# Kernel tuning notes

Hardware: AMD Instinct MI355X
Metric: run time of the kernel (lower is better)

Reference implementation:

```python
import jax, jax.numpy as jnp
import numpy as np
import math

B, T, C, TF, N, DK = 4, 2048, 768, 128, 8, 96  # DK = max(C//8,16)

def _tau_init(Tw):
    alpha = 0.1 ** (1.0 / max(Tw - 1, 1))
    tau = -math.log(max(alpha, 1e-10))
    return math.log(math.exp(tau) - 1 + 1e-10)

def setup_inputs() -> dict:
    key = jax.random.key(0)
    ks = jax.random.split(key, 13)
    w = lambda k, shp: jax.random.normal(k, shp, jnp.float32) * 0.02
    return {
        'x': jax.random.normal(ks[0], (B, T, C), jnp.float32),
        'tau_gate': jnp.float32(_tau_init(max(T // 2, 4))),
        'tau_fast': jnp.float32(_tau_init(TF)),
        'tau_slow': jnp.float32(_tau_init(T)),
        'Wp': w(ks[1], (C, C)), 'bp': jnp.zeros((C,), jnp.float32),
        'Wxf': w(ks[2], (C, C)), 'bxf': jnp.full((C,), -0.5, jnp.float32),
        'Wxs': w(ks[3], (C, C)), 'bxs': jnp.full((C,), 0.5, jnp.float32),
        'Wcf': w(ks[4], (C, C)), 'Wcs': w(ks[5], (C, C)),
        'Wq': w(ks[6], (DK, C)), 'Wk': w(ks[7], (DK, C)),
        'Wfast': w(ks[8], (C, C)), 'bfast': jnp.zeros((C,), jnp.float32),
        'Wslow': w(ks[9], (C, C)), 'bslow': jnp.zeros((C,), jnp.float32),
        'Wsoma': w(ks[10], (C, C)), 'bsoma': jnp.zeros((C,), jnp.float32),
        'Wanc': w(ks[11], (C, C)), 'banc': jnp.zeros((C,), jnp.float32),
        'anchor_scales': jnp.linspace(1.5, -1.5, N).astype(jnp.float32),
        'blend_raw': jnp.zeros((1,), jnp.float32),
        'ln_g': jnp.ones((C,), jnp.float32), 'ln_b': jnp.zeros((C,), jnp.float32),
    }

def _lin(x, W, b=None):
    # torch Linear: y = x @ W.T + b, W is (out, in)
    y = jnp.einsum('btc,oc->bto', x, W)
    return y if b is None else y + b

def _ema(b, tau_raw):
    # exact h_t = alpha*h_{t-1} + b_t, h_{-1}=0 (same math as full causal conv with kernel alpha^j)
    alpha = jnp.exp(-jax.nn.softplus(tau_raw))
    def step(h, bt):
        h = alpha * h + bt
        return h, h
    _, hs = jax.lax.scan(step, jnp.zeros_like(b[:, 0, :]), jnp.swapaxes(b, 0, 1))
    return jnp.swapaxes(hs, 0, 1)  # (B,T,C)

def _forward(x, tau_gate, tau_fast, tau_slow, Wp, bp, Wxf, bxf, Wxs, bxs, Wcf, Wcs,
             Wq, Wk, Wfast, bfast, Wslow, bslow, Wsoma, bsoma, Wanc, banc,
             anchor_scales, blend_raw, ln_g, ln_b):
    x_proj = jnp.tanh(_lin(x, Wp, bp))
    ctx_gate = _ema(x, tau_gate)
    wg_f = jax.nn.sigmoid(_lin(x, Wxf, bxf) + _lin(ctx_gate, Wcf))
    wg_s = jax.nn.sigmoid(_lin(x, Wxs, bxs) + _lin(ctx_gate, Wcs))
    ctx_fast = _ema(x_proj * wg_f, tau_fast)
    ctx_slow = _ema(x_proj * wg_s, tau_slow)
    # F1 content gate: causal max-score sigmoid
    q = _lin(x, Wq)
    k = _lin(x, Wk)
    sc = jnp.einsum('btd,bsd->bts', q, k) * (DK ** -0.5)
    tril = jnp.tril(jnp.ones((T, T), bool))
    sc = jnp.where(tril[None], sc, -jnp.inf)
    cg = jax.nn.sigmoid(jnp.max(sc, axis=-1, keepdims=True))  # (B,T,1)
    ctx_fast = ctx_fast * cg
    ctx_slow = ctx_slow * cg
    # F5 anchors (static positions)
    pos = np.array([min(i * (T // N), T - 1) for i in range(N)])
    a = jnp.tanh(jnp.einsum('bnc,oc->bno', x[:, pos, :], Wanc) + banc)  # (B,N,C)
    delta = jnp.einsum('n,bnc->bc', jax.nn.sigmoid(anchor_scales), a)
    ctx_fast = ctx_fast + delta[:, None, :]
    ctx_slow = ctx_slow + delta[:, None, :]
    # F6 blend of fast/slow gates (torch.lerp)
    bl = jax.nn.sigmoid(blend_raw)  # (1,)
    gf = jax.nn.sigmoid(_lin(ctx_fast, Wfast, bfast))
    gs = jax.nn.sigmoid(_lin(ctx_slow, Wslow, bslow))
    gate = gf + bl * (gs - gf)
    soma = jnp.tanh(_lin(x, Wsoma, bsoma))
    y = soma * gate
    mu = jnp.mean(y, -1, keepdims=True)
    var = jnp.var(y, -1, keepdims=True)
    return (y - mu) / jnp.sqrt(var + 1e-5) * ln_g + ln_b  # dropout p=0 -> identity

def reference(x, tau_gate, tau_fast, tau_slow, Wp, bp, Wxf, bxf, Wxs, bxs, Wcf, Wcs,
              Wq, Wk, Wfast, bfast, Wslow, bslow, Wsoma, bsoma, Wanc, banc,
              anchor_scales, blend_raw, ln_g, ln_b):
    return _forward(x, tau_gate, tau_fast, tau_slow, Wp, bp, Wxf, bxf, Wxs, bxs, Wcf, Wcs,
                    Wq, Wk, Wfast, bfast, Wslow, bslow, Wsoma, bsoma, Wanc, banc,
                    anchor_scales, blend_raw, ln_g, ln_b)
```

## Files before the change

### kernel.cpp

```cpp
#include <hip/hip_runtime.h>
#include <math.h>

#define B_ 4
#define T_ 2048
#define C_ 768
#define DK_ 96
#define NA_ 8
#define M_ (B_*T_)
#define K2_ (2*C_)
#define NCH_ 256
#define CK_ 8

typedef __attribute__((ext_vector_type(8))) _Float16 half8;
typedef __attribute__((ext_vector_type(4))) _Float16 half4;
typedef __attribute__((ext_vector_type(4))) float floatx4;

#define AS1 __attribute__((address_space(1)))
#define AS3 __attribute__((address_space(3)))

__device__ __forceinline__ float sigm(float x){ return 1.f/(1.f + expf(-x)); }
__device__ __forceinline__ unsigned enc_max(float f){
  unsigned i = __float_as_uint(f);
  return (i & 0x80000000u) ? ~i : (i | 0x80000000u);
}
__device__ __forceinline__ float dec_max(unsigned u){
  unsigned i = (u & 0x80000000u) ? (u & 0x7FFFFFFFu) : ~u;
  return __uint_as_float(i);
}
__device__ __forceinline__ void gld16(const _Float16* g, _Float16* l){
  __builtin_amdgcn_global_load_lds((const AS1 unsigned int*)g, (AS3 unsigned int*)l, 16, 0, 0);
}

#define NB0 4608
#define NB1 4896
#define NB2 5920
#define NB3 5944
__global__ __launch_bounds__(256) void k_prep(
    const float* __restrict__ x,
    const float* __restrict__ Wp, const float* __restrict__ Wfast,
    const float* __restrict__ Wslow, const float* __restrict__ Wsoma,
    const float* __restrict__ Wxf, const float* __restrict__ Wxs,
    const float* __restrict__ Wcf, const float* __restrict__ Wcs,
    const float* __restrict__ Wq, const float* __restrict__ Wk,
    const float* __restrict__ Wanc, const float* __restrict__ banc,
    const float* __restrict__ ascl, const float* __restrict__ tau_gate,
    _Float16* __restrict__ wall, _Float16* __restrict__ wqk,
    unsigned* __restrict__ cgE, _Float16* __restrict__ xh,
    float* __restrict__ Sg, float* __restrict__ dlt)
{
  __shared__ float xs[NA_*C_];
  __shared__ float part[NA_*128];
  int blk = blockIdx.x, tid = threadIdx.x;
  if (blk < NB0){
    int i = blk*256 + tid;
    const int per = (C_*C_)/4;
    int s = i / per, j = i - s*per;
    const float* src = s==0?Wp : s==1?Wfast : s==2?Wslow : s==3?Wsoma
                     : s==4?Wxf : s==5?Wxs : s==6?Wcf : Wcs;
    float4 v = ((const float4*)src)[j];
    half4 h = { (_Float16)v.x, (_Float16)v.y, (_Float16)v.z, (_Float16)v.w };
    ((half4*)wall)[(size_t)s*per + j] = h;
  } else if (blk < NB1){
    int sub = blk - NB0;
    if (sub >= 256){ cgE[(sub-256)*256 + tid] = 0u; return; }
    const float* src = (sub < 96) ? Wq + (size_t)sub*C_
                     : (sub < 192 ? Wk + (size_t)(sub-96)*C_ : nullptr);
    #pragma unroll
    for (int k = 0; k < 3; ++k){
      int c = tid + k*256;
      wqk[(size_t)sub*C_ + c] = src ? (_Float16)src[c] : (_Float16)0.f;
    }
  } else if (blk < NB2){
    if (tid >= 192) return;
    int sub = blk - NB1;
    float al = expf(-log1pf(expf(tau_gate[0])));
    int b = sub >> 8, ch = sub & (NCH_-1);
    int t0 = b*T_ + ch*CK_;
    float s0=0.f,s1=0.f,s2=0.f,s3=0.f;
    #pragma unroll
    for (int t = 0; t < CK_; ++t){
      float4 v = *(const float4*)(x + (size_t)(t0+t)*C_ + tid*4);
      half4 h = { (_Float16)v.x,(_Float16)v.y,(_Float16)v.z,(_Float16)v.w };
      *(half4*)(xh + (size_t)(t0+t)*C_ + tid*4) = h;
      s0 = al*s0 + v.x; s1 = al*s1 + v.y; s2 = al*s2 + v.z; s3 = al*s3 + v.w;
    }
    float4 sv = { s0,s1,s2,s3 };
    *(float4*)(Sg + (size_t)sub*C_ + tid*4) = sv;
  } else {
    int ab = blk - NB2;
    int ct = ab % 6, b = ab / 6;
    for (int i = tid; i < NA_*C_; i += 256){
      int n = i / C_, c = i - n*C_;
      xs[i] = x[(size_t)(b*T_ + n*(T_/NA_))*C_ + c];
    }
    __syncthreads();
    int col = ct*128 + (tid & 127), kh = tid >> 7;
    float acc[NA_] = {0,0,0,0,0,0,0,0};
    const float* wrow = Wanc + (size_t)col*C_ + kh*384;
    const float* xk = xs + kh*384;
    for (int k = 0; k < 384; ++k){
      float wv = wrow[k];
      #pragma unroll
      for (int n = 0; n < NA_; ++n) acc[n] += xk[n*C_ + k]*wv;
    }
    if (kh){
      #pragma unroll
      for (int n = 0; n < NA_; ++n) part[n*128 + (tid & 127)] = acc[n];
    }
    __syncthreads();
    if (!kh){
      float d = 0.f;
      float bv = banc[col];
      #pragma unroll
      for (int n = 0; n < NA_; ++n){
        float a = tanhf(acc[n] + part[n*128 + (tid & 127)] + bv);
        d += sigm(ascl[n]) * a;
      }
      dlt[(size_t)b*C_ + col] = d;
    }
  }
}

__global__ __launch_bounds__(256) void k_p2_gate(const float* __restrict__ S, float* __restrict__ H,
                                                 const float* __restrict__ tau){
  int blk = blockIdx.x;
  int b = blk / 3, c = (blk - b*3)*256 + threadIdx.x;
  float aCK = expf(-(float)CK_ * log1pf(expf(tau[0])));
  float h = 0.f;
  for (int ch = 0; ch < NCH_; ++ch){
    size_t idx = (size_t)(b*NCH_ + ch)*C_ + c;
    H[idx] = h;
    h = aCK*h + S[idx];
  }
}

__global__ __launch_bounds__(256) void k_p2_fs(const float* __restrict__ Sf, const float* __restrict__ Ss,
                                               float* __restrict__ Hf, float* __restrict__ Hs,
                                               const float* __restrict__ tf, const float* __restrict__ ts){
  int blk = blockIdx.x;
  int which = blk / 12, sub = blk - which*12;
  int b = sub / 3, c = (sub - b*3)*256 + threadIdx.x;
  const float* S = which ? Ss : Sf;
  float* H = which ? Hs : Hf;
  float aCK = expf(-(float)CK_ * log1pf(expf(which ? ts[0] : tf[0])));
  float h = 0.f;
  for (int ch = 0; ch < NCH_; ++ch){
    size_t idx = (size_t)(b*NCH_ + ch)*C_ + c;
    H[idx] = h;
    h = aCK*h + S[idx];
  }
}

__global__ __launch_bounds__(192) void k_gate_p3(
    const _Float16* __restrict__ xh, const float* __restrict__ H,
    const float* __restrict__ tau, _Float16* __restrict__ gate){
  float al = expf(-log1pf(expf(tau[0])));
  int blk = blockIdx.x, b = blk >> 8, ch = blk & (NCH_-1);
  int c4 = threadIdx.x;
  float4 h0 = *(const float4*)(H + (size_t)blk*C_ + c4*4);
  float g0=h0.x, g1=h0.y, g2=h0.z, g3=h0.w;
  int t0 = b*T_ + ch*CK_;
  #pragma unroll
  for (int t = 0; t < CK_; ++t){
    half4 v = *(const half4*)(xh + (size_t)(t0+t)*C_ + c4*4);
    g0 = al*g0 + (float)v[0]; g1 = al*g1 + (float)v[1];
    g2 = al*g2 + (float)v[2]; g3 = al*g3 + (float)v[3];
    half4 o = { (_Float16)g0,(_Float16)g1,(_Float16)g2,(_Float16)g3 };
    *(half4*)(gate + (size_t)(t0+t)*C_ + c4*4) = o;
  }
}

__device__ __forceinline__ void stage_tile(const _Float16* __restrict__ src, int stride,
                                           int r0, int k0, _Float16* lds){
  int tid = threadIdx.x;
  int wave = tid >> 6, lane = tid & 63;
  #pragma unroll
  for (int it = 0; it < 4; ++it){
    int cb = it*256 + wave*64;
    int ck = cb + lane;
    int row = ck >> 3;
    int kp = (ck & 7) ^ (row & 7);
    gld16(src + (size_t)(r0+row)*stride + k0 + kp*8, lds + (size_t)cb*8);
  }
}

__device__ __forceinline__ void mfma_pass(const _Float16* As, const _Float16* Ws, floatx4 acc[4][4]){
  int tid = threadIdx.x;
  int wave = tid >> 6, lane = tid & 63;
  int wr = wave >> 1, wc = wave & 1;
  int lr = lane & 15, lq = lane >> 4;
  #pragma unroll
  for (int ks = 0; ks < 2; ++ks){
    half8 fa[4], fb[4];
    int off = (((ks*4 + lq) ^ (lr & 7)) << 3);
    #pragma unroll
    for (int i = 0; i < 4; ++i){
      fa[i] = *(const half8*)(As + (wr*64 + i*16 + lr)*64 + off);
      fb[i] = *(const half8*)(Ws + (wc*64 + i*16 + lr)*64 + off);
    }
    #pragma unroll
    for (int i = 0; i < 4; ++i)
      #pragma unroll
      for (int j = 0; j < 4; ++j)
        acc[i][j] = __builtin_amdgcn_mfma_f32_16x16x32_f16(fa[i], fb[j], acc[i][j], 0, 0, 0);
  }
}

__device__ __forceinline__ void store_tile_f16(floatx4 acc[4][4], _Float16* __restrict__ out, int ldo,
                                               const float* bias, const float* bias2,
                                               int m0, int n0, int act){
  int tid = threadIdx.x;
  int wave = tid >> 6, lane = tid & 63;
  int wr = wave >> 1, wc = wave & 1;
  int lr = lane & 15, lq = lane >> 4;
  #pragma unroll
  for (int i = 0; i < 4; ++i){
    #pragma unroll
    for (int j = 0; j < 4; ++j){
      int col = n0 + wc*64 + j*16 + lr;
      float bv = 0.f;
      if (bias) bv = (bias2 && col >= C_) ? bias2[col - C_] : bias[col];
      #pragma unroll
      for (int r = 0; r < 4; ++r){
        int rowm = m0 + wr*64 + i*16 + lq*4 + r;
        float z = acc[i][j][r] + bv;
        if (act == 1) z = tanhf(z);
        else if (act == 2) z = sigm(z);
        out[(size_t)rowm*ldo + col] = (_Float16)z;
      }
    }
  }
}

__global__ __launch_bounds__(256,4) void k_gemm_s3(
    const _Float16* __restrict__ xh, const _Float16* __restrict__ gate,
    const _Float16* __restrict__ wall, const _Float16* __restrict__ wqk,
    const float* __restrict__ bp, const float* __restrict__ bxf, const float* __restrict__ bxs,
    _Float16* __restrict__ xph, _Float16* __restrict__ wgfs, _Float16* __restrict__ qk)
{
  __shared__ _Float16 As[128*64];
  __shared__ _Float16 Ws[128*64];
  const size_t per = (size_t)C_*C_;
  floatx4 acc[4][4] = {};
  int m0 = blockIdx.x * 128;
  int ny = blockIdx.y;
  if (ny < 6){
    for (int k0 = 0; k0 < C_; k0 += 64){
      stage_tile(xh, C_, m0, k0, As);
      stage_tile(wall, C_, ny*128, k0, Ws);
      asm volatile("s_waitcnt vmcnt(0)" ::: "memory");
      __syncthreads();
      mfma_pass(As, Ws, acc);
      __syncthreads();
    }
    store_tile_f16(acc, xph, C_, bp, nullptr, m0, ny*128, 1);
  } else if (ny < 18){
    int n0 = (ny-6)*128;
    for (int k0 = 0; k0 < C_; k0 += 64){
      stage_tile(xh, C_, m0, k0, As);
      stage_tile(wall + 4*per, C_, n0, k0, Ws);
      asm volatile("s_waitcnt vmcnt(0)" ::: "memory");
      __syncthreads();
      mfma_pass(As, Ws, acc);
      __syncthreads();
    }
    for (int k0 = 0; k0 < C_; k0 += 64){
      stage_tile(gate, C_, m0, k0, As);
      stage_tile(wall + 6*per, C_, n0, k0, Ws);
      asm volatile("s_waitcnt vmcnt(0)" ::: "memory");
      __syncthreads();
      mfma_pass(As, Ws, acc);
      __syncthreads();
    }
    store_tile_f16(acc, wgfs, K2_, bxf, bxs, m0, n0, 2);
  } else {
    int n0 = (ny-18)*128;
    for (int k0 = 0; k0 < C_; k0 += 64){
      stage_tile(xh, C_, m0, k0, As);
      stage_tile(wqk, C_, n0, k0, Ws);
      asm volatile("s_waitcnt vmcnt(0)" ::: "memory");
      __syncthreads();
      mfma_pass(As, Ws, acc);
      __syncthreads();
    }
    store_tile_f16(acc, qk, 256, nullptr, nullptr, m0, n0, 0);
  }
}

__global__ __launch_bounds__(256,3) void k_gemm_s7(
    const _Float16* __restrict__ xph, const _Float16* __restrict__ wgfs,
    const _Float16* __restrict__ xh, const _Float16* __restrict__ wall,
    const float* __restrict__ Hf, const float* __restrict__ Hs,
    const float* __restrict__ tau_fast, const float* __restrict__ tau_slow,
    const unsigned* __restrict__ cgE, const float* __restrict__ dlt,
    const float* __restrict__ bf, const float* __restrict__ bs, const float* __restrict__ bso,
    _Float16* __restrict__ gfb, _Float16* __restrict__ gsb, _Float16* __restrict__ somab)
{
  __shared__ _Float16 As[128*64];
  __shared__ _Float16 Wg[128*64];
  __shared__ _Float16 Bs[128*64];
  __shared__ float cgv[128];
  const size_t per = (size_t)C_*C_;
  floatx4 acc[4][4] = {};
  int m0 = blockIdx.x * 128;
  int s = blockIdx.y / 6, nt = (blockIdx.y % 6) * 128;
  int tid = threadIdx.x;
  if (s == 2){
    for (int k0 = 0; k0 < C_; k0 += 64){
      stage_tile(xh, C_, m0, k0, As);
      stage_tile(wall + 3*per, C_, nt, k0, Bs);
      asm volatile("s_waitcnt vmcnt(0)" ::: "memory");
      __syncthreads();
      mfma_pass(As, Bs, acc);
      __syncthreads();
    }
    store_tile_f16(acc, somab, C_, bso, nullptr, m0, nt, 1);
  } else {
    float al = expf(-log1pf(expf(s ? tau_slow[0] : tau_fast[0])));
    const float* Hx = s ? Hs : Hf;
    const _Float16* wsrc = wgfs + (s ? C_ : 0);
    const _Float16* Wm = wall + (size_t)(s+1)*per;
    int b = m0 >> 11;
    int ch0 = (m0 & (T_-1)) >> 3;
    if (tid < 128) cgv[tid] = sigm(dec_max(cgE[m0 + tid]));
    __syncthreads();
    int rc = tid >> 4, cc = (tid >> 1) & 7, hh = tid & 1;
    for (int k0 = 0; k0 < C_; k0 += 64){
      stage_tile(xph, C_, m0, k0, As);
      stage_tile(wsrc, K2_, m0, k0, Wg);
      stage_tile(Wm, C_, nt, k0, Bs);
      asm volatile("s_waitcnt vmcnt(0)" ::: "memory");
      __syncthreads();
      {
        float4 hv = *(const float4*)(Hx + ((size_t)b*NCH_ + ch0 + rc)*C_ + k0 + cc*8 + hh*4);
        float4 d  = *(const float4*)(dlt + (size_t)b*C_ + k0 + cc*8 + hh*4);
        float e0=hv.x, e1=hv.y, e2=hv.z, e3=hv.w;
        #pragma unroll
        for (int r = 0; r < 8; ++r){
          int idx = (rc*8+r)*64 + ((cc^r)<<3) + hh*4;
          half4 p = *(const half4*)(As+idx);
          half4 wv = *(const half4*)(Wg+idx);
          e0 = al*e0 + (float)p[0]*(float)wv[0];
          e1 = al*e1 + (float)p[1]*(float)wv[1];
          e2 = al*e2 + (float)p[2]*(float)wv[2];
          e3 = al*e3 + (float)p[3]*(float)wv[3];
          float cgr = cgv[rc*8 + r];
          half4 o = { (_Float16)(e0*cgr + d.x), (_Float16)(e1*cgr + d.y),
                      (_Float16)(e2*cgr + d.z), (_Float16)(e3*cgr + d.w) };
          *(half4*)(As+idx) = o;
        }
      }
      __syncthreads();
      mfma_pass(As, Bs, acc);
      __syncthreads();
    }
    store_tile_f16(acc, s ? gsb : gfb, C_, s ? bs : bf, nullptr, m0, nt, 2);
  }
}

#define SLDK 104
__global__ __launch_bounds__(256,2) void k_score_fs(
    const _Float16* __restrict__ qk, unsigned* __restrict__ cgE,
    const _Float16* __restrict__ xp, const _Float16* __restrict__ wgfs,
    const float* __restrict__ tf, const float* __restrict__ ts,
    float* __restrict__ Sf, float* __restrict__ Ss)
{
  __shared__ _Float16 Qs[128*SLDK];
  __shared__ _Float16 Ks[128*SLDK];
  __shared__ float sred[256];
  int idx = blockIdx.x;
  int tid = threadIdx.x;
  if (idx >= 544){
    if (tid >= 192) return;
    int f = idx - 544;
    float af = expf(-log1pf(expf(tf[0])));
    float as = expf(-log1pf(expf(ts[0])));
    int b = f >> 8, ch = f & (NCH_-1);
    int t0 = b*T_ + ch*CK_;
    float f0=0,f1=0,f2=0,f3=0, s0=0,s1=0,s2=0,s3=0;
    #pragma unroll
    for (int t = 0; t < CK_; ++t){
      half4 p = *(const half4*)(xp + (size_t)(t0+t)*C_ + tid*4);
      half4 wf = *(const half4*)(wgfs + (size_t)(t0+t)*K2_ + tid*4);
      half4 ws = *(const half4*)(wgfs + (size_t)(t0+t)*K2_ + C_ + tid*4);
      f0 = af*f0 + (float)p[0]*(float)wf[0]; s0 = as*s0 + (float)p[0]*(float)ws[0];
      f1 = af*f1 + (float)p[1]*(float)wf[1]; s1 = as*s1 + (float)p[1]*(float)ws[1];
      f2 = af*f2 + (float)p[2]*(float)wf[2]; s2 = as*s2 + (float)p[2]*(float)ws[2];
      f3 = af*f3 + (float)p[3]*(float)wf[3]; s3 = as*s3 + (float)p[3]*(float)ws[3];
    }
    float4 fv = { f0,f1,f2,f3 }, sv = { s0,s1,s2,s3 };
    *(float4*)(Sf + (size_t)f*C_ + tid*4) = fv;
    *(float4*)(Ss + (size_t)f*C_ + tid*4) = sv;
    return;
  }
  int b = idx / 136;
  int p = idx - b*136;
  int ti = (int)((sqrtf(8.f*p + 1.f) - 1.f)*0.5f);
  while ((ti+1)*(ti+2)/2 <= p) ++ti;
  while (ti*(ti+1)/2 > p) --ti;
  int sj = p - ti*(ti+1)/2;

  const _Float16* qg = qk + (size_t)(b*T_ + ti*128)*256;
  const _Float16* kg = qk + (size_t)(b*T_ + sj*128)*256 + 96;
  #pragma unroll
  for (int r = 0; r < 6; ++r){
    int ci = tid + r*256;
    int row = ci / 12, kp = ci % 12;
    *(uint4*)(&Qs[row*SLDK + kp*8]) = *(const uint4*)(qg + (size_t)row*256 + kp*8);
    *(uint4*)(&Ks[row*SLDK + kp*8]) = *(const uint4*)(kg + (size_t)row*256 + kp*8);
  }
  __syncthreads();

  int wave = tid >> 6, lane = tid & 63;
  int wr = wave >> 1, wc = wave & 1;
  int lr = lane & 15, lq = lane >> 4;
  floatx4 acc[4][4] = {};
  #pragma unroll
  for (int ks = 0; ks < 3; ++ks){
    half8 fa[4], fb[4];
    #pragma unroll
    for (int i = 0; i < 4; ++i){
      fa[i] = *(const half8*)(&Qs[(wr*64 + i*16 + lr)*SLDK + ks*32 + lq*8]);
      fb[i] = *(const half8*)(&Ks[(wc*64 + i*16 + lr)*SLDK + ks*32 + lq*8]);
    }
    #pragma unroll
    for (int i = 0; i < 4; ++i)
      #pragma unroll
      for (int j = 0; j < 4; ++j)
        acc[i][j] = __builtin_amdgcn_mfma_f32_16x16x32_f16(fa[i], fb[j], acc[i][j], 0, 0, 0);
  }
  const float scale = 0.10206207f;
  #pragma unroll
  for (int i = 0; i < 4; ++i){
    #pragma unroll
    for (int r = 0; r < 4; ++r){
      int row64 = i*16 + lq*4 + r;
      int tg = ti*128 + wr*64 + row64;
      float v = -3.0e38f;
      #pragma unroll
      for (int j = 0; j < 4; ++j){
        int sg = sj*128 + wc*64 + j*16 + lr;
        if (sg <= tg) v = fmaxf(v, acc[i][j][r]*scale);
      }
      #pragma unroll
      for (int off = 1; off < 16; off <<= 1) v = fmaxf(v, __shfl_xor(v, off, 16));
      if (lr == 0) sred[wr*128 + wc*64 + row64] = v;
    }
  }
  __syncthreads();
  if (wc == 0 && lane < 64){
    int row64 = lane;
    float v = fmaxf(sred[wr*128 + row64], sred[wr*128 + 64 + row64]);
    int tg = ti*128 + wr*64 + row64;
    atomicMax(&cgE[(size_t)b*T_ + tg], enc_max(v));
  }
}

__global__ __launch_bounds__(192) void k_ln(const _Float16* __restrict__ gfb,
                                            const _Float16* __restrict__ gsb,
                                            const _Float16* __restrict__ somab,
                                            const float* __restrict__ blendr,
                                            const float* __restrict__ g, const float* __restrict__ be,
                                            float* __restrict__ out){
  int row = blockIdx.x;
  int tid = threadIdx.x;
  float bl = sigm(blendr[0]);
  size_t base = (size_t)row*C_ + tid*4;
  half4 gf4 = *(const half4*)(gfb + base);
  half4 gs4 = *(const half4*)(gsb + base);
  half4 so4 = *(const half4*)(somab + base);
  float v[4];
  #pragma unroll
  for (int i = 0; i < 4; ++i){
    float gf = (float)gf4[i], gs = (float)gs4[i], so = (float)so4[i];
    v[i] = so * (gf + bl*(gs - gf));
  }
  float s = v[0]+v[1]+v[2]+v[3];
  float ss = v[0]*v[0]+v[1]*v[1]+v[2]*v[2]+v[3]*v[3];
  #pragma unroll
  for (int off = 1; off < 64; off <<= 1){ s += __shfl_xor(s, off); ss += __shfl_xor(ss, off); }
  __shared__ float sb[6];
  int wave = tid >> 6, lane = tid & 63;
  if (lane == 0){ sb[wave] = s; sb[3+wave] = ss; }
  __syncthreads();
  s  = sb[0]+sb[1]+sb[2];
  ss = sb[3]+sb[4]+sb[5];
  float mu  = s * (1.f/C_);
  float var = ss * (1.f/C_) - mu*mu;
  float inv = rsqrtf(var + 1e-5f);
  float4 o;
  o.x = (v[0]-mu)*inv*g[tid*4+0] + be[tid*4+0];
  o.y = (v[1]-mu)*inv*g[tid*4+1] + be[tid*4+1];
  o.z = (v[2]-mu)*inv*g[tid*4+2] + be[tid*4+2];
  o.w = (v[3]-mu)*inv*g[tid*4+3] + be[tid*4+3];
  *(float4*)(out + base) = o;
}

extern "C" void kernel_launch(void* const* d_in, const int* in_sizes, int n_in,
                              void* d_out, int out_size, void* d_ws, size_t ws_size,
                              hipStream_t stream){
  (void)in_sizes; (void)n_in; (void)out_size;
  const float* x        = (const float*)d_in[0];
  const float* tau_gate = (const float*)d_in[1];
  const float* tau_fast = (const float*)d_in[2];
  const float* tau_slow = (const float*)d_in[3];
  const float* Wp   = (const float*)d_in[4];  const float* bp    = (const float*)d_in[5];
  const float* Wxf  = (const float*)d_in[6];  const float* bxf   = (const float*)d_in[7];
  const float* Wxs  = (const float*)d_in[8];  const float* bxs   = (const float*)d_in[9];
  const float* Wcf  = (const float*)d_in[10]; const float* Wcs   = (const float*)d_in[11];
  const float* Wq   = (const float*)d_in[12]; const float* Wk    = (const float*)d_in[13];
  const float* Wfast= (const float*)d_in[14]; const float* bfast = (const float*)d_in[15];
  const float* Wslow= (const float*)d_in[16]; const float* bslow = (const float*)d_in[17];
  const float* Wsoma= (const float*)d_in[18]; const float* bsoma = (const float*)d_in[19];
  const float* Wanc = (const float*)d_in[20]; const float* banc  = (const float*)d_in[21];
  const float* ascl = (const float*)d_in[22]; const float* blendr= (const float*)d_in[23];
  const float* lng  = (const float*)d_in[24]; const float* lnb   = (const float*)d_in[25];
  float* out = (float*)d_out;

  char* w = (char*)d_ws;
  auto alloc = [&](size_t bytes)->void*{
    void* p = (void*)w; w += (bytes + 255) & ~(size_t)255; return p;
  };
  _Float16* xh    = (_Float16*)alloc((size_t)M_*C_*2);
  _Float16* wall  = (_Float16*)alloc((size_t)8*C_*C_*2);
  _Float16* wqk   = (_Float16*)alloc((size_t)256*C_*2);
  _Float16* xph   = (_Float16*)alloc((size_t)M_*C_*2);
  _Float16* wgfs  = (_Float16*)alloc((size_t)M_*K2_*2);
  _Float16* qk    = (_Float16*)alloc((size_t)M_*256*2);
  _Float16* gfb   = (_Float16*)alloc((size_t)M_*C_*2);
  _Float16* gsb   = (_Float16*)alloc((size_t)M_*C_*2);
  _Float16* somab = (_Float16*)alloc((size_t)M_*C_*2);
  unsigned* cgE   = (unsigned*)alloc((size_t)M_*4);
  float* Sg = (float*)alloc((size_t)B_*NCH_*C_*4);
  float* Hg = (float*)alloc((size_t)B_*NCH_*C_*4);
  float* Ss = (float*)alloc((size_t)B_*NCH_*C_*4);
  float* Hs = (float*)alloc((size_t)B_*NCH_*C_*4);
  float* dlt = (float*)alloc((size_t)B_*C_*4);
  _Float16* gate = gfb;
  float* Sf = Sg;
  float* Hf = Hg;
  if ((size_t)(w - (char*)d_ws) > ws_size) return;

  k_prep<<<NB3, 256, 0, stream>>>(x, Wp, Wfast, Wslow, Wsoma, Wxf, Wxs, Wcf, Wcs, Wq, Wk,
                                  Wanc, banc, ascl, tau_gate, wall, wqk, cgE, xh, Sg, dlt);
  k_p2_gate<<<B_*3, 256, 0, stream>>>(Sg, Hg, tau_gate);
  k_gate_p3<<<B_*NCH_, 192, 0, stream>>>(xh, Hg, tau_gate, gate);
  k_gemm_s3<<<dim3(M_/128, 20), 256, 0, stream>>>(xh, gate, wall, wqk,
                                                  bp, bxf, bxs, xph, wgfs, qk);
  k_score_fs<<<544 + B_*NCH_, 256, 0, stream>>>(qk, cgE, xph, wgfs, tau_fast, tau_slow, Sf, Ss);
  k_p2_fs<<<2*B_*3, 256, 0, stream>>>(Sf, Ss, Hf, Hs, tau_fast, tau_slow);
  k_gemm_s7<<<dim3(M_/128, 18), 256, 0, stream>>>(xph, wgfs, xh, wall, Hf, Hs,
                                                  tau_fast, tau_slow, cgE, dlt,
                                                  bfast, bslow, bsoma, gfb, gsb, somab);
  k_ln<<<M_, 192, 0, stream>>>(gfb, gsb, somab, blendr, lng, lnb, out);
}
```

Measured before the change: 388.4 us.

## Reshuffle prep kernels, raise score occupancy, one-wave-per-row layernorm

The x cast and chunk-EMA work moves out of k_prep into its own kernel. The serial gate carry-scan (k_p2_gate) becomes extra blocks of k_prep, so the launch count stays the same and the scan now overlaps with the weight casting. k_score_fs asks for 3 blocks per CU instead of 2, which may force register spills. LayerNorm now processes one row per wave, four rows per block, reducing only with shuffles and no shared-memory sync.

```diff
diff --git a/kernel.cpp b/kernel.cpp
--- a/kernel.cpp
+++ b/kernel.cpp
@@ -31,10 +31,29 @@
   __builtin_amdgcn_global_load_lds((const AS1 unsigned int*)g, (AS3 unsigned int*)l, 16, 0, 0);
 }
 
+__global__ __launch_bounds__(192) void k_castx(
+    const float* __restrict__ x, const float* __restrict__ tau,
+    _Float16* __restrict__ xh, float* __restrict__ Sg){
+  float al = expf(-log1pf(expf(tau[0])));
+  int blk = blockIdx.x, b = blk >> 8, ch = blk & (NCH_-1);
+  int t0 = b*T_ + ch*CK_;
+  int c4 = threadIdx.x;
+  float s0=0.f,s1=0.f,s2=0.f,s3=0.f;
+  #pragma unroll
+  for (int t = 0; t < CK_; ++t){
+    float4 v = *(const float4*)(x + (size_t)(t0+t)*C_ + c4*4);
+    half4 h = { (_Float16)v.x,(_Float16)v.y,(_Float16)v.z,(_Float16)v.w };
+    *(half4*)(xh + (size_t)(t0+t)*C_ + c4*4) = h;
+    s0 = al*s0 + v.x; s1 = al*s1 + v.y; s2 = al*s2 + v.z; s3 = al*s3 + v.w;
+  }
+  float4 sv = { s0,s1,s2,s3 };
+  *(float4*)(Sg + (size_t)blk*C_ + c4*4) = sv;
+}
+
 #define NB0 4608
 #define NB1 4896
-#define NB2 5920
-#define NB3 5944
+#define NB2 4920
+#define NB3 4932
 __global__ __launch_bounds__(256) void k_prep(
     const float* __restrict__ x,
     const float* __restrict__ Wp, const float* __restrict__ Wfast,
@@ -44,9 +63,9 @@
     const float* __restrict__ Wq, const float* __restrict__ Wk,
     const float* __restrict__ Wanc, const float* __restrict__ banc,
     const float* __restrict__ ascl, const float* __restrict__ tau_gate,
+    const float* __restrict__ Sg,
     _Float16* __restrict__ wall, _Float16* __restrict__ wqk,
-    unsigned* __restrict__ cgE, _Float16* __restrict__ xh,
-    float* __restrict__ Sg, float* __restrict__ dlt)
+    unsigned* __restrict__ cgE, float* __restrict__ Hg, float* __restrict__ dlt)
 {
   __shared__ float xs[NA_*C_];
   __shared__ float part[NA_*128];
@@ -71,23 +90,7 @@
       wqk[(size_t)sub*C_ + c] = src ? (_Float16)src[c] : (_Float16)0.f;
     }
   } else if (blk < NB2){
-    if (tid >= 192) return;
-    int sub = blk - NB1;
-    float al = expf(-log1pf(expf(tau_gate[0])));
-    int b = sub >> 8, ch = sub & (NCH_-1);
-    int t0 = b*T_ + ch*CK_;
-    float s0=0.f,s1=0.f,s2=0.f,s3=0.f;
-    #pragma unroll
-    for (int t = 0; t < CK_; ++t){
-      float4 v = *(const float4*)(x + (size_t)(t0+t)*C_ + tid*4);
-      half4 h = { (_Float16)v.x,(_Float16)v.y,(_Float16)v.z,(_Float16)v.w };
-      *(half4*)(xh + (size_t)(t0+t)*C_ + tid*4) = h;
-      s0 = al*s0 + v.x; s1 = al*s1 + v.y; s2 = al*s2 + v.z; s3 = al*s3 + v.w;
-    }
-    float4 sv = { s0,s1,s2,s3 };
-    *(float4*)(Sg + (size_t)sub*C_ + tid*4) = sv;
-  } else {
-    int ab = blk - NB2;
+    int ab = blk - NB1;
     int ct = ab % 6, b = ab / 6;
     for (int i = tid; i < NA_*C_; i += 256){
       int n = i / C_, c = i - n*C_;
@@ -118,19 +121,16 @@
       }
       dlt[(size_t)b*C_ + col] = d;
     }
-  }
-}
-
-__global__ __launch_bounds__(256) void k_p2_gate(const float* __restrict__ S, float* __restrict__ H,
-                                                 const float* __restrict__ tau){
-  int blk = blockIdx.x;
-  int b = blk / 3, c = (blk - b*3)*256 + threadIdx.x;
-  float aCK = expf(-(float)CK_ * log1pf(expf(tau[0])));
-  float h = 0.f;
-  for (int ch = 0; ch < NCH_; ++ch){
-    size_t idx = (size_t)(b*NCH_ + ch)*C_ + c;
-    H[idx] = h;
-    h = aCK*h + S[idx];
+  } else {
+    int sub = blk - NB2;
+    int b = sub / 3, c = (sub - b*3)*256 + tid;
+    float aCK = expf(-(float)CK_ * log1pf(expf(tau_gate[0])));
+    float h = 0.f;
+    for (int ch = 0; ch < NCH_; ++ch){
+      size_t idx = (size_t)(b*NCH_ + ch)*C_ + c;
+      Hg[idx] = h;
+      h = aCK*h + Sg[idx];
+    }
   }
 }
 
@@ -359,7 +359,7 @@
 }
 
 #define SLDK 104
-__global__ __launch_bounds__(256,2) void k_score_fs(
+__global__ __launch_bounds__(256,3) void k_score_fs(
     const _Float16* __restrict__ qk, unsigned* __restrict__ cgE,
     const _Float16* __restrict__ xp, const _Float16* __restrict__ wgfs,
     const float* __restrict__ tf, const float* __restrict__ ts,
@@ -456,44 +456,46 @@
   }
 }
 
-__global__ __launch_bounds__(192) void k_ln(const _Float16* __restrict__ gfb,
+__global__ __launch_bounds__(256) void k_ln(const _Float16* __restrict__ gfb,
                                             const _Float16* __restrict__ gsb,
                                             const _Float16* __restrict__ somab,
                                             const float* __restrict__ blendr,
                                             const float* __restrict__ g, const float* __restrict__ be,
                                             float* __restrict__ out){
-  int row = blockIdx.x;
-  int tid = threadIdx.x;
+  int wave = threadIdx.x >> 6, lane = threadIdx.x & 63;
+  int row = blockIdx.x*4 + wave;
   float bl = sigm(blendr[0]);
-  size_t base = (size_t)row*C_ + tid*4;
-  half4 gf4 = *(const half4*)(gfb + base);
-  half4 gs4 = *(const half4*)(gsb + base);
-  half4 so4 = *(const half4*)(somab + base);
-  float v[4];
-  #pragma unroll
-  for (int i = 0; i < 4; ++i){
-    float gf = (float)gf4[i], gs = (float)gs4[i], so = (float)so4[i];
-    v[i] = so * (gf + bl*(gs - gf));
-  }
-  float s = v[0]+v[1]+v[2]+v[3];
-  float ss = v[0]*v[0]+v[1]*v[1]+v[2]*v[2]+v[3]*v[3];
+  size_t rb = (size_t)row*C_;
+  float v[12];
+  float s = 0.f, ss = 0.f;
+  #pragma unroll
+  for (int w2 = 0; w2 < 3; ++w2){
+    size_t o = rb + w2*256 + lane*4;
+    half4 gf4 = *(const half4*)(gfb + o);
+    half4 gs4 = *(const half4*)(gsb + o);
+    half4 so4 = *(const half4*)(somab + o);
+    #pragma unroll
+    for (int i = 0; i < 4; ++i){
+      float gf = (float)gf4[i], gs = (float)gs4[i], so = (float)so4[i];
+      float y = so * (gf + bl*(gs - gf));
+      v[w2*4 + i] = y; s += y; ss += y*y;
+    }
+  }
   #pragma unroll
   for (int off = 1; off < 64; off <<= 1){ s += __shfl_xor(s, off); ss += __shfl_xor(ss, off); }
-  __shared__ float sb[6];
-  int wave = tid >> 6, lane = tid & 63;
-  if (lane == 0){ sb[wave] = s; sb[3+wave] = ss; }
-  __syncthreads();
-  s  = sb[0]+sb[1]+sb[2];
-  ss = sb[3]+sb[4]+sb[5];
   float mu  = s * (1.f/C_);
   float var = ss * (1.f/C_) - mu*mu;
   float inv = rsqrtf(var + 1e-5f);
-  float4 o;
-  o.x = (v[0]-mu)*inv*g[tid*4+0] + be[tid*4+0];
-  o.y = (v[1]-mu)*inv*g[tid*4+1] + be[tid*4+1];
-  o.z = (v[2]-mu)*inv*g[tid*4+2] + be[tid*4+2];
-  o.w = (v[3]-mu)*inv*g[tid*4+3] + be[tid*4+3];
-  *(float4*)(out + base) = o;
+  #pragma unroll
+  for (int w2 = 0; w2 < 3; ++w2){
+    int c0 = w2*256 + lane*4;
+    float4 o4;
+    o4.x = (v[w2*4+0]-mu)*inv*g[c0+0] + be[c0+0];
+    o4.y = (v[w2*4+1]-mu)*inv*g[c0+1] + be[c0+1];
+    o4.z = (v[w2*4+2]-mu)*inv*g[c0+2] + be[c0+2];
+    o4.w = (v[w2*4+3]-mu)*inv*g[c0+3] + be[c0+3];
+    *(float4*)(out + rb + c0) = o4;
+  }
 }
 
 extern "C" void kernel_launch(void* const* d_in, const int* in_sizes, int n_in,
@@ -541,9 +543,9 @@
   float* Hf = Hg;
   if ((size_t)(w - (char*)d_ws) > ws_size) return;
 
+  k_castx<<<B_*NCH_, 192, 0, stream>>>(x, tau_gate, xh, Sg);
   k_prep<<<NB3, 256, 0, stream>>>(x, Wp, Wfast, Wslow, Wsoma, Wxf, Wxs, Wcf, Wcs, Wq, Wk,
-                                  Wanc, banc, ascl, tau_gate, wall, wqk, cgE, xh, Sg, dlt);
-  k_p2_gate<<<B_*3, 256, 0, stream>>>(Sg, Hg, tau_gate);
+                                  Wanc, banc, ascl, tau_gate, Sg, wall, wqk, cgE, Hg, dlt);
   k_gate_p3<<<B_*NCH_, 192, 0, stream>>>(xh, Hg, tau_gate, gate);
   k_gemm_s3<<<dim3(M_/128, 20), 256, 0, stream>>>(xh, gate, wall, wqk,
                                                   bp, bxf, bxs, xph, wgfs, qk);
@@ -552,5 +554,5 @@
   k_gemm_s7<<<dim3(M_/128, 18), 256, 0, stream>>>(xph, wgfs, xh, wall, Hf, Hs,
                                                   tau_fast, tau_slow, cgE, dlt,
                                                   bfast, bslow, bsoma, gfb, gsb, somab);
-  k_ln<<<M_, 192, 0, stream>>>(gfb, gsb, somab, blendr, lng, lnb, out);
-}
+  k_ln<<<M_/4, 256, 0, stream>>>(gfb, gsb, somab, blendr, lng, lnb, out);
+}
```

Result: faster. 351.6 us (-9.5%).
